# Kernel optimization log

Hardware: AMD Instinct MI355X
Metric: run time of the kernel (lower is better)

Reference implementation:

```python
import jax, jax.numpy as jnp
import numpy as np

B, H, W = 4, 64, 1024
h, w = 32, 512
K = 16
C = 64
EPS = 1e-5


def setup_inputs() -> dict:
    key = jax.random.key(0)
    ks = jax.random.split(key, 8)
    n_sampled = h * w
    xyz_proj = jax.random.normal(ks[0], (B, H, W, 3), dtype=jnp.float32)
    points_proj = jax.random.normal(ks[1], (B, H, W, C), dtype=jnp.float32)
    xyz_sampled_proj = jax.random.normal(ks[2], (B, h, w, 3), dtype=jnp.float32)
    # Precomputed neighbor selection (stand-in for fused_conv_random_k, which is
    # a non-differentiable custom CUDA op producing detached indices + mask).
    neighbor_idx = jax.random.randint(ks[3], (B, n_sampled * K), 0, H * W, dtype=jnp.int32)
    valid_mask = (jax.random.uniform(ks[4], (B, n_sampled, K, 1)) > 0.1).astype(jnp.float32)
    # 1x1 conv MLP params (torch Conv2d weight (out,in,1,1) stored here as (in,out))
    def mk(k, cin, cout):
        kw, = jax.random.split(k, 1)
        wgt = jax.random.normal(kw, (cin, cout), dtype=jnp.float32) * (1.0 / np.sqrt(cin))
        return wgt
    w0 = mk(ks[5], 3 + C, 64)
    w1 = mk(ks[6], 64, 64)
    w2 = mk(ks[7], 64, 128)
    z = lambda c: jnp.zeros((c,), jnp.float32)
    o = lambda c: jnp.ones((c,), jnp.float32)
    return dict(
        xyz_proj=xyz_proj, points_proj=points_proj, xyz_sampled_proj=xyz_sampled_proj,
        neighbor_idx=neighbor_idx, valid_mask=valid_mask,
        w0=w0, b0=z(64), g0=o(64), be0=z(64), m0=z(64), v0=o(64),
        w1=w1, b1=z(64), g1=o(64), be1=z(64), m1=z(64), v1=o(64),
        w2=w2, b2=z(128), g2=o(128), be2=z(128), m2=z(128), v2=o(128),
    )


def _conv_bn_relu(x, wgt, b, g, be, m, v):
    # 1x1 conv == matmul over channel dim; BN in eval mode with running stats.
    y = jnp.einsum('bnkc,co->bnko', x, wgt) + b
    y = g * (y - m) * jax.lax.rsqrt(v + EPS) + be
    return jax.nn.relu(y)


def reference(xyz_proj, points_proj, xyz_sampled_proj, neighbor_idx, valid_mask,
              w0, b0, g0, be0, m0, v0,
              w1, b1, g1, be1, m1, v1,
              w2, b2, g2, be2, m2, v2):
    Bc = xyz_proj.shape[0]
    Cc = points_proj.shape[3]
    hh, ww = xyz_sampled_proj.shape[1], xyz_sampled_proj.shape[2]
    n_sampled = hh * ww
    xyz_bn3 = xyz_proj.reshape(Bc, -1, 3)          # (B, H*W, 3)
    points_bnc = points_proj.reshape(Bc, -1, Cc)   # (B, H*W, C)
    idx = neighbor_idx[..., None]                  # (B, n*K, 1)
    new_xyz_group = jnp.take_along_axis(xyz_bn3, idx, axis=1).reshape(Bc, n_sampled, K, 3)
    new_points_group = jnp.take_along_axis(points_bnc, idx, axis=1).reshape(Bc, n_sampled, K, Cc)
    new_xyz_group = new_xyz_group * valid_mask
    new_points_group = new_points_group * valid_mask
    new_xyz = xyz_sampled_proj.reshape(Bc, n_sampled, 1, 3)
    xyz_diff = new_xyz_group - new_xyz             # broadcast over K
    feat = jnp.concatenate([xyz_diff, new_points_group], axis=-1)  # (B, n, K, 3+C)
    feat = _conv_bn_relu(feat, w0, b0, g0, be0, m0, v0)
    feat = _conv_bn_relu(feat, w1, b1, g1, be1, m1, v1)
    feat = _conv_bn_relu(feat, w2, b2, g2, be2, m2, v2)
    points_down_sample = jnp.max(feat, axis=2)     # (B, n, 128) max-pool over K
    points_down_sample_proj = points_down_sample.reshape(Bc, hh, ww, -1)
    return points_down_sample, points_down_sample_proj
```

## Files before the change

kernel.cpp:

```cpp
#include <hip/hip_runtime.h>


#define NGRP_    16384
#define OUTHALF_ 8388608
#define WS_      72
#define XS2_     36
#define EPS_     1e-5f
#define GRID_    1024

typedef _Float16 h8    __attribute__((ext_vector_type(8)));
typedef float    f32x4 __attribute__((ext_vector_type(4)));
typedef unsigned u32x2 __attribute__((ext_vector_type(2)));

__global__ __launch_bounds__(256) void cvt_pts_kernel(
    const float* __restrict__ src, _Float16* __restrict__ dst)
{
    const size_t i = ((size_t)blockIdx.x * 256 + threadIdx.x) * 8;
    f32x4 a = *(const f32x4*)(src + i);
    f32x4 b = *(const f32x4*)(src + i + 4);
    h8 o;
#pragma unroll
    for (int j = 0; j < 4; ++j) { o[j] = (_Float16)a[j]; o[4 + j] = (_Float16)b[j]; }
    *(h8*)(dst + i) = o;
}

#define PK(lo, hi) ({                                                          \
    const _Float16 _l = (_Float16)fmaxf((lo), 0.f);                            \
    const _Float16 _h = (_Float16)fmaxf((hi), 0.f);                            \
    (unsigned)__builtin_bit_cast(unsigned short, _l) |                         \
    ((unsigned)__builtin_bit_cast(unsigned short, _h) << 16); })

template<bool PRE>
__device__ __forceinline__ void load_pt(const void* __restrict__ ptsv,
                                        size_t row, int quad, h8& o0, h8& o1)
{
    if constexpr (PRE) {
        const _Float16* pw = (const _Float16*)ptsv + (row << 6);
        o0 = *(const h8*)(pw + quad * 8);
        o1 = *(const h8*)(pw + 32 + quad * 8);
    } else {
        const float* pw = (const float*)ptsv + (row << 6);
        f32x4 r0 = *(const f32x4*)(pw + quad * 8);
        f32x4 r1 = *(const f32x4*)(pw + quad * 8 + 4);
        f32x4 r2 = *(const f32x4*)(pw + 32 + quad * 8);
        f32x4 r3 = *(const f32x4*)(pw + 32 + quad * 8 + 4);
#pragma unroll
        for (int j = 0; j < 4; ++j) { o0[j]=(_Float16)r0[j]; o0[4+j]=(_Float16)r1[j];
                                      o1[j]=(_Float16)r2[j]; o1[4+j]=(_Float16)r3[j]; }
    }
}

template<bool PRE>
__global__ __launch_bounds__(256, 4) void pnsa_main(
    const float* __restrict__ xyz,
    const void*  __restrict__ ptsv,
    const float* __restrict__ xyzs,
    const int*   __restrict__ nidx,
    const float* __restrict__ vmask,
    const float* __restrict__ w0, const float* __restrict__ b0,
    const float* __restrict__ g0, const float* __restrict__ be0,
    const float* __restrict__ m0, const float* __restrict__ v0,
    const float* __restrict__ w1, const float* __restrict__ b1,
    const float* __restrict__ g1, const float* __restrict__ be1,
    const float* __restrict__ m1, const float* __restrict__ v1,
    const float* __restrict__ w2, const float* __restrict__ b2,
    const float* __restrict__ g2, const float* __restrict__ be2,
    const float* __restrict__ m2, const float* __restrict__ v2,
    float*       __restrict__ out)
{
    __shared__ __align__(16) _Float16 ldsW1[64 * WS_];
    __shared__ __align__(16) _Float16 ldsW2[128 * WS_];
    __shared__ __align__(16) float    t1sh[64];
    __shared__ __align__(16) float    t2sh[128];
    __shared__ __align__(16) unsigned ldsX[4][16 * XS2_];

    const int tid  = threadIdx.x;
    const int wave = tid >> 6;
    const int lane = tid & 63;
    const int l15  = lane & 15;
    const int quad = lane >> 4;

    unsigned* Xp = &ldsX[wave][0];

    if (tid < 64) {
        const float s = g1[tid] * rsqrtf(v1[tid] + EPS_);
        t1sh[tid] = (b1[tid] - m1[tid]) * s + be1[tid];
    }
    if (tid < 128) {
        const float s = g2[tid] * rsqrtf(v2[tid] + EPS_);
        t2sh[tid] = (b2[tid] - m2[tid]) * s + be2[tid];
    }
    for (int idx = tid; idx < 64 * 64; idx += 256) {
        const int k = idx >> 6, n = idx & 63;
        ldsW1[n * WS_ + k] = (_Float16)(w1[idx] * (g1[n] * rsqrtf(v1[n] + EPS_)));
    }
    for (int idx = tid; idx < 64 * 128; idx += 256) {
        const int k = idx >> 7, n = idx & 127;
        ldsW2[n * WS_ + k] = (_Float16)(w2[idx] * (g2[n] * rsqrtf(v2[n] + EPS_)));
    }
    __syncthreads();

    h8 b0f[4][3];
#pragma unroll
    for (int nt = 0; nt < 4; ++nt) {
        const int ch = nt * 16 + l15;
        const float s = g0[ch] * rsqrtf(v0[ch] + EPS_);
        const float t0 = (b0[ch] - m0[ch]) * s + be0[ch];
#pragma unroll
        for (int kk = 0; kk < 3; ++kk) {
            h8 f;
#pragma unroll
            for (int j = 0; j < 8; ++j) {
                const int k = kk * 32 + quad * 8 + j;
                float wv = 0.f;
                if (k < 64)       wv = w0[(3 + k) * 64 + ch] * s;
                else if (k < 67)  wv = w0[(k - 64) * 64 + ch] * s;
                else if (k == 67) wv = t0;
                f[j] = (_Float16)wv;
            }
            b0f[nt][kk] = f;
        }
    }

    h8 q0, q1;
    float xg0, xg1, xg2, xs0, xs1, xs2, mk;
    int nb_nxt;
    {
        const int p = (blockIdx.x << 2) + wave;
        const int nb0 = nidx[(p << 4) + l15];
        const size_t row = (size_t)(((p >> 14) << 16) + nb0);
        load_pt<PRE>(ptsv, row, quad, q0, q1);
        const float* xgp = xyz + row * 3;
        xg0 = xgp[0]; xg1 = xgp[1]; xg2 = xgp[2];
        mk = vmask[(p << 4) + l15];
        const float* xsp = xyzs + (size_t)p * 3;
        xs0 = xsp[0]; xs1 = xsp[1]; xs2 = xsp[2];
        const int g1i = (blockIdx.x + GRID_ < NGRP_) ? blockIdx.x + GRID_ : blockIdx.x;
        nb_nxt = nidx[(((g1i << 2) + wave) << 4) + l15];
    }

    for (int grp = blockIdx.x; grp < NGRP_; grp += GRID_) {
        const int p = (grp << 2) + wave;
        const int gn  = (grp + GRID_ < NGRP_) ? grp + GRID_ : grp;
        const int gnn = (gn + GRID_ < NGRP_) ? gn + GRID_ : gn;
        const int pn  = (gn << 2) + wave;

        const size_t rowN = (size_t)(((pn >> 14) << 16) + nb_nxt);
        h8 q0n, q1n;
        load_pt<PRE>(ptsv, rowN, quad, q0n, q1n);
        const float* xgpn = xyz + rowN * 3;
        const float xg0n = xgpn[0], xg1n = xgpn[1], xg2n = xgpn[2];
        const float mkn = vmask[(pn << 4) + l15];
        const float* xspn = xyzs + (size_t)pn * 3;
        const float xs0n = xspn[0], xs1n = xspn[1], xs2n = xspn[2];
        const int nb_n2 = nidx[(((gnn << 2) + wave) << 4) + l15];

        h8 a0 = q0, a1 = q1;
        if (mk == 0.0f) { a0 = (h8)(_Float16)0.f; a1 = (h8)(_Float16)0.f; }
        h8 a2 = (h8)(_Float16)0.f;
        if (quad == 0) {
            a2[0] = (_Float16)(xg0 * mk - xs0);
            a2[1] = (_Float16)(xg1 * mk - xs1);
            a2[2] = (_Float16)(xg2 * mk - xs2);
            a2[3] = (_Float16)1.0f;
        }

#pragma unroll
        for (int nt = 0; nt < 4; ++nt) {
            f32x4 acc = {0.f, 0.f, 0.f, 0.f};
            acc = __builtin_amdgcn_mfma_f32_16x16x32_f16(b0f[nt][0], a0, acc, 0, 0, 0);
            acc = __builtin_amdgcn_mfma_f32_16x16x32_f16(b0f[nt][1], a1, acc, 0, 0, 0);
            acc = __builtin_amdgcn_mfma_f32_16x16x32_f16(b0f[nt][2], a2, acc, 0, 0, 0);
            u32x2 pk = {PK(acc[0], acc[1]), PK(acc[2], acc[3])};
            *(u32x2*)(Xp + l15 * XS2_ + nt * 8 + quad * 2) = pk;
        }

        h8 x0 = *(const h8*)(Xp + l15 * XS2_ + quad * 4);
        h8 x1 = *(const h8*)(Xp + l15 * XS2_ + 16 + quad * 4);
#pragma unroll 2
        for (int nt = 0; nt < 4; ++nt) {
            const _Float16* wrow = ldsW1 + (nt * 16 + l15) * WS_ + quad * 8;
            h8 wa = *(const h8*)(wrow);
            h8 wb = *(const h8*)(wrow + 32);
            const f32x4 t1 = *(const f32x4*)(t1sh + nt * 16 + quad * 4);
            f32x4 acc = t1;
            acc = __builtin_amdgcn_mfma_f32_16x16x32_f16(wa, x0, acc, 0, 0, 0);
            acc = __builtin_amdgcn_mfma_f32_16x16x32_f16(wb, x1, acc, 0, 0, 0);
            u32x2 pk = {PK(acc[0], acc[1]), PK(acc[2], acc[3])};
            *(u32x2*)(Xp + l15 * XS2_ + nt * 8 + quad * 2) = pk;
        }

        h8 y0 = *(const h8*)(Xp + l15 * XS2_ + quad * 4);
        h8 y1 = *(const h8*)(Xp + l15 * XS2_ + 16 + quad * 4);
        float* ob = out + ((size_t)p << 7);
#pragma unroll 2
        for (int nt = 0; nt < 8; ++nt) {
            const _Float16* wrow = ldsW2 + (nt * 16 + l15) * WS_ + quad * 8;
            h8 wa = *(const h8*)(wrow);
            h8 wb = *(const h8*)(wrow + 32);
            const float t2 = t2sh[nt * 16 + l15];
            f32x4 acc = {0.f, 0.f, 0.f, 0.f};
            acc = __builtin_amdgcn_mfma_f32_16x16x32_f16(y0, wa, acc, 0, 0, 0);
            acc = __builtin_amdgcn_mfma_f32_16x16x32_f16(y1, wb, acc, 0, 0, 0);
            float v = fmaxf(fmaxf(acc[0], acc[1]), fmaxf(acc[2], acc[3])) + t2;
            v = fmaxf(v, 0.f);
            v = fmaxf(v, __shfl_xor(v, 16, 64));
            v = fmaxf(v, __shfl_xor(v, 32, 64));
            if (quad == 0) {
                ob[nt * 16 + l15]            = v;
                ob[OUTHALF_ + nt * 16 + l15] = v;
            }
        }

        q0 = q0n; q1 = q1n;
        xg0 = xg0n; xg1 = xg1n; xg2 = xg2n;
        xs0 = xs0n; xs1 = xs1n; xs2 = xs2n;
        mk = mkn; nb_nxt = nb_n2;
    }
}

extern "C" void kernel_launch(void* const* d_in, const int* in_sizes, int n_in,
                              void* d_out, int out_size, void* d_ws, size_t ws_size,
                              hipStream_t stream) {
    const float* xyz   = (const float*)d_in[0];
    const float* pts   = (const float*)d_in[1];
    const float* xyzs  = (const float*)d_in[2];
    const int*   nidx  = (const int*)d_in[3];
    const float* vmask = (const float*)d_in[4];
    const float *w0 = (const float*)d_in[5],  *b0 = (const float*)d_in[6],
                *g0 = (const float*)d_in[7],  *be0 = (const float*)d_in[8],
                *m0 = (const float*)d_in[9],  *v0 = (const float*)d_in[10];
    const float *w1 = (const float*)d_in[11], *b1 = (const float*)d_in[12],
                *g1 = (const float*)d_in[13], *be1 = (const float*)d_in[14],
                *m1 = (const float*)d_in[15], *v1 = (const float*)d_in[16];
    const float *w2 = (const float*)d_in[17], *b2 = (const float*)d_in[18],
                *g2 = (const float*)d_in[19], *be2 = (const float*)d_in[20],
                *m2 = (const float*)d_in[21], *v2 = (const float*)d_in[22];
    float* outp = (float*)d_out;

    const size_t PTS_ELEMS = 16777216ull;
    if (ws_size >= PTS_ELEMS * sizeof(_Float16)) {
        _Float16* ptsh = (_Float16*)d_ws;
        cvt_pts_kernel<<<dim3(8192), dim3(256), 0, stream>>>(pts, ptsh);
        pnsa_main<true><<<dim3(GRID_), dim3(256), 0, stream>>>(
            xyz, (const void*)ptsh, xyzs, nidx, vmask,
            w0, b0, g0, be0, m0, v0,
            w1, b1, g1, be1, m1, v1,
            w2, b2, g2, be2, m2, v2, outp);
    } else {
        pnsa_main<false><<<dim3(GRID_), dim3(256), 0, stream>>>(
            xyz, (const void*)pts, xyzs, nidx, vmask,
            w0, b0, g0, be0, m0, v0,
            w1, b1, g1, be1, m1, v1,
            w2, b2, g2, be2, m2, v2, outp);
    }
}
```

Baseline: 227.6 us.

## Hoist layer-1/2 weight fragments into registers and drop point-data software prefetch

Loads all W1/W2 MFMA fragments and bias vectors from LDS into registers once per block instead of re-reading them every group iteration. To make room, it drops the one-iteration-ahead prefetch of gathered point and xyz data (only the neighbor index is still prefetched), lowers launch bounds to 2 blocks per CU and halves the persistent grid. It also replaces the manual fp16 packing with the packed cvt_pkrtz conversion and precomputes BN scales once in shared memory. The trade is fewer LDS reads per group against lower occupancy and less latency hiding for the random gather loads.

```diff
diff --git a/kernel.cpp b/kernel.cpp
--- a/kernel.cpp
+++ b/kernel.cpp
@@ -6,9 +6,10 @@
 #define WS_      72
 #define XS2_     36
 #define EPS_     1e-5f
-#define GRID_    1024
+#define GRID_    512
 
 typedef _Float16 h8    __attribute__((ext_vector_type(8)));
+typedef _Float16 h2    __attribute__((ext_vector_type(2)));
 typedef float    f32x4 __attribute__((ext_vector_type(4)));
 typedef unsigned u32x2 __attribute__((ext_vector_type(2)));
 
@@ -24,34 +25,11 @@
     *(h8*)(dst + i) = o;
 }
 
-#define PK(lo, hi) ({                                                          \
-    const _Float16 _l = (_Float16)fmaxf((lo), 0.f);                            \
-    const _Float16 _h = (_Float16)fmaxf((hi), 0.f);                            \
-    (unsigned)__builtin_bit_cast(unsigned short, _l) |                         \
-    ((unsigned)__builtin_bit_cast(unsigned short, _h) << 16); })
+#define PK2(lo, hi) __builtin_bit_cast(unsigned,                               \
+    __builtin_amdgcn_cvt_pkrtz(fmaxf((lo), 0.f), fmaxf((hi), 0.f)))
 
 template<bool PRE>
-__device__ __forceinline__ void load_pt(const void* __restrict__ ptsv,
-                                        size_t row, int quad, h8& o0, h8& o1)
-{
-    if constexpr (PRE) {
-        const _Float16* pw = (const _Float16*)ptsv + (row << 6);
-        o0 = *(const h8*)(pw + quad * 8);
-        o1 = *(const h8*)(pw + 32 + quad * 8);
-    } else {
-        const float* pw = (const float*)ptsv + (row << 6);
-        f32x4 r0 = *(const f32x4*)(pw + quad * 8);
-        f32x4 r1 = *(const f32x4*)(pw + quad * 8 + 4);
-        f32x4 r2 = *(const f32x4*)(pw + 32 + quad * 8);
-        f32x4 r3 = *(const f32x4*)(pw + 32 + quad * 8 + 4);
-#pragma unroll
-        for (int j = 0; j < 4; ++j) { o0[j]=(_Float16)r0[j]; o0[4+j]=(_Float16)r1[j];
-                                      o1[j]=(_Float16)r2[j]; o1[4+j]=(_Float16)r3[j]; }
-    }
-}
-
-template<bool PRE>
-__global__ __launch_bounds__(256, 4) void pnsa_main(
+__global__ __launch_bounds__(256, 2) void pnsa_main(
     const float* __restrict__ xyz,
     const void*  __restrict__ ptsv,
     const float* __restrict__ xyzs,
@@ -70,8 +48,8 @@
 {
     __shared__ __align__(16) _Float16 ldsW1[64 * WS_];
     __shared__ __align__(16) _Float16 ldsW2[128 * WS_];
-    __shared__ __align__(16) float    t1sh[64];
-    __shared__ __align__(16) float    t2sh[128];
+    __shared__ __align__(16) float    s1sh[64], t1sh[64];
+    __shared__ __align__(16) float    s2sh[128], t2sh[128];
     __shared__ __align__(16) unsigned ldsX[4][16 * XS2_];
 
     const int tid  = threadIdx.x;
@@ -84,21 +62,45 @@
 
     if (tid < 64) {
         const float s = g1[tid] * rsqrtf(v1[tid] + EPS_);
+        s1sh[tid] = s;
         t1sh[tid] = (b1[tid] - m1[tid]) * s + be1[tid];
     }
     if (tid < 128) {
         const float s = g2[tid] * rsqrtf(v2[tid] + EPS_);
+        s2sh[tid] = s;
         t2sh[tid] = (b2[tid] - m2[tid]) * s + be2[tid];
     }
+    __syncthreads();
     for (int idx = tid; idx < 64 * 64; idx += 256) {
         const int k = idx >> 6, n = idx & 63;
-        ldsW1[n * WS_ + k] = (_Float16)(w1[idx] * (g1[n] * rsqrtf(v1[n] + EPS_)));
+        ldsW1[n * WS_ + k] = (_Float16)(w1[idx] * s1sh[n]);
     }
     for (int idx = tid; idx < 64 * 128; idx += 256) {
         const int k = idx >> 7, n = idx & 127;
-        ldsW2[n * WS_ + k] = (_Float16)(w2[idx] * (g2[n] * rsqrtf(v2[n] + EPS_)));
+        ldsW2[n * WS_ + k] = (_Float16)(w2[idx] * s2sh[n]);
     }
     __syncthreads();
+
+    h8 w1f[4][2], w2f[8][2];
+#pragma unroll
+    for (int nt = 0; nt < 4; ++nt) {
+        const _Float16* wrow = ldsW1 + (nt * 16 + l15) * WS_ + quad * 8;
+        w1f[nt][0] = *(const h8*)(wrow);
+        w1f[nt][1] = *(const h8*)(wrow + 32);
+    }
+#pragma unroll
+    for (int nt = 0; nt < 8; ++nt) {
+        const _Float16* wrow = ldsW2 + (nt * 16 + l15) * WS_ + quad * 8;
+        w2f[nt][0] = *(const h8*)(wrow);
+        w2f[nt][1] = *(const h8*)(wrow + 32);
+    }
+    f32x4 t1v[4];
+#pragma unroll
+    for (int nt = 0; nt < 4; ++nt)
+        t1v[nt] = *(const f32x4*)(t1sh + nt * 16 + quad * 4);
+    float t2v[8];
+#pragma unroll
+    for (int nt = 0; nt < 8; ++nt) t2v[nt] = t2sh[nt * 16 + l15];
 
     h8 b0f[4][3];
 #pragma unroll
@@ -122,41 +124,37 @@
         }
     }
 
-    h8 q0, q1;
-    float xg0, xg1, xg2, xs0, xs1, xs2, mk;
-    int nb_nxt;
-    {
-        const int p = (blockIdx.x << 2) + wave;
-        const int nb0 = nidx[(p << 4) + l15];
-        const size_t row = (size_t)(((p >> 14) << 16) + nb0);
-        load_pt<PRE>(ptsv, row, quad, q0, q1);
-        const float* xgp = xyz + row * 3;
-        xg0 = xgp[0]; xg1 = xgp[1]; xg2 = xgp[2];
-        mk = vmask[(p << 4) + l15];
-        const float* xsp = xyzs + (size_t)p * 3;
-        xs0 = xsp[0]; xs1 = xsp[1]; xs2 = xsp[2];
-        const int g1i = (blockIdx.x + GRID_ < NGRP_) ? blockIdx.x + GRID_ : blockIdx.x;
-        nb_nxt = nidx[(((g1i << 2) + wave) << 4) + l15];
-    }
+    int nb = nidx[((((blockIdx.x) << 2) + wave) << 4) + l15];
 
     for (int grp = blockIdx.x; grp < NGRP_; grp += GRID_) {
         const int p = (grp << 2) + wave;
-        const int gn  = (grp + GRID_ < NGRP_) ? grp + GRID_ : grp;
-        const int gnn = (gn + GRID_ < NGRP_) ? gn + GRID_ : gn;
-        const int pn  = (gn << 2) + wave;
-
-        const size_t rowN = (size_t)(((pn >> 14) << 16) + nb_nxt);
-        h8 q0n, q1n;
-        load_pt<PRE>(ptsv, rowN, quad, q0n, q1n);
-        const float* xgpn = xyz + rowN * 3;
-        const float xg0n = xgpn[0], xg1n = xgpn[1], xg2n = xgpn[2];
-        const float mkn = vmask[(pn << 4) + l15];
-        const float* xspn = xyzs + (size_t)pn * 3;
-        const float xs0n = xspn[0], xs1n = xspn[1], xs2n = xspn[2];
-        const int nb_n2 = nidx[(((gnn << 2) + wave) << 4) + l15];
-
-        h8 a0 = q0, a1 = q1;
-        if (mk == 0.0f) { a0 = (h8)(_Float16)0.f; a1 = (h8)(_Float16)0.f; }
+        const int gn = (grp + GRID_ < NGRP_) ? grp + GRID_ : grp;
+        const int pn = (gn << 2) + wave;
+
+        const size_t row = (size_t)(((p >> 14) << 16) + nb);
+        h8 q0, q1;
+        if constexpr (PRE) {
+            const _Float16* pw = (const _Float16*)ptsv + (row << 6);
+            q0 = *(const h8*)(pw + quad * 8);
+            q1 = *(const h8*)(pw + 32 + quad * 8);
+        } else {
+            const float* pw = (const float*)ptsv + (row << 6);
+            f32x4 r0 = *(const f32x4*)(pw + quad * 8);
+            f32x4 r1 = *(const f32x4*)(pw + quad * 8 + 4);
+            f32x4 r2 = *(const f32x4*)(pw + 32 + quad * 8);
+            f32x4 r3 = *(const f32x4*)(pw + 32 + quad * 8 + 4);
+#pragma unroll
+            for (int j = 0; j < 4; ++j) { q0[j]=(_Float16)r0[j]; q0[4+j]=(_Float16)r1[j];
+                                          q1[j]=(_Float16)r2[j]; q1[4+j]=(_Float16)r3[j]; }
+        }
+        const float mk = vmask[(p << 4) + l15];
+        const float* xgp = xyz + row * 3;
+        const float xg0 = xgp[0], xg1 = xgp[1], xg2 = xgp[2];
+        const float* xsp = xyzs + (size_t)p * 3;
+        const float xs0 = xsp[0], xs1 = xsp[1], xs2 = xsp[2];
+        const int nb_n = nidx[(pn << 4) + l15];
+
+        if (mk == 0.0f) { q0 = (h8)(_Float16)0.f; q1 = (h8)(_Float16)0.f; }
         h8 a2 = (h8)(_Float16)0.f;
         if (quad == 0) {
             a2[0] = (_Float16)(xg0 * mk - xs0);
@@ -168,41 +166,33 @@
 #pragma unroll
         for (int nt = 0; nt < 4; ++nt) {
             f32x4 acc = {0.f, 0.f, 0.f, 0.f};
-            acc = __builtin_amdgcn_mfma_f32_16x16x32_f16(b0f[nt][0], a0, acc, 0, 0, 0);
-            acc = __builtin_amdgcn_mfma_f32_16x16x32_f16(b0f[nt][1], a1, acc, 0, 0, 0);
+            acc = __builtin_amdgcn_mfma_f32_16x16x32_f16(b0f[nt][0], q0, acc, 0, 0, 0);
+            acc = __builtin_amdgcn_mfma_f32_16x16x32_f16(b0f[nt][1], q1, acc, 0, 0, 0);
             acc = __builtin_amdgcn_mfma_f32_16x16x32_f16(b0f[nt][2], a2, acc, 0, 0, 0);
-            u32x2 pk = {PK(acc[0], acc[1]), PK(acc[2], acc[3])};
+            u32x2 pk = {PK2(acc[0], acc[1]), PK2(acc[2], acc[3])};
             *(u32x2*)(Xp + l15 * XS2_ + nt * 8 + quad * 2) = pk;
         }
 
         h8 x0 = *(const h8*)(Xp + l15 * XS2_ + quad * 4);
         h8 x1 = *(const h8*)(Xp + l15 * XS2_ + 16 + quad * 4);
-#pragma unroll 2
+#pragma unroll
         for (int nt = 0; nt < 4; ++nt) {
-            const _Float16* wrow = ldsW1 + (nt * 16 + l15) * WS_ + quad * 8;
-            h8 wa = *(const h8*)(wrow);
-            h8 wb = *(const h8*)(wrow + 32);
-            const f32x4 t1 = *(const f32x4*)(t1sh + nt * 16 + quad * 4);
-            f32x4 acc = t1;
-            acc = __builtin_amdgcn_mfma_f32_16x16x32_f16(wa, x0, acc, 0, 0, 0);
-            acc = __builtin_amdgcn_mfma_f32_16x16x32_f16(wb, x1, acc, 0, 0, 0);
-            u32x2 pk = {PK(acc[0], acc[1]), PK(acc[2], acc[3])};
+            f32x4 acc = t1v[nt];
+            acc = __builtin_amdgcn_mfma_f32_16x16x32_f16(w1f[nt][0], x0, acc, 0, 0, 0);
+            acc = __builtin_amdgcn_mfma_f32_16x16x32_f16(w1f[nt][1], x1, acc, 0, 0, 0);
+            u32x2 pk = {PK2(acc[0], acc[1]), PK2(acc[2], acc[3])};
             *(u32x2*)(Xp + l15 * XS2_ + nt * 8 + quad * 2) = pk;
         }
 
         h8 y0 = *(const h8*)(Xp + l15 * XS2_ + quad * 4);
         h8 y1 = *(const h8*)(Xp + l15 * XS2_ + 16 + quad * 4);
         float* ob = out + ((size_t)p << 7);
-#pragma unroll 2
+#pragma unroll
         for (int nt = 0; nt < 8; ++nt) {
-            const _Float16* wrow = ldsW2 + (nt * 16 + l15) * WS_ + quad * 8;
-            h8 wa = *(const h8*)(wrow);
-            h8 wb = *(const h8*)(wrow + 32);
-            const float t2 = t2sh[nt * 16 + l15];
             f32x4 acc = {0.f, 0.f, 0.f, 0.f};
-            acc = __builtin_amdgcn_mfma_f32_16x16x32_f16(y0, wa, acc, 0, 0, 0);
-            acc = __builtin_amdgcn_mfma_f32_16x16x32_f16(y1, wb, acc, 0, 0, 0);
-            float v = fmaxf(fmaxf(acc[0], acc[1]), fmaxf(acc[2], acc[3])) + t2;
+            acc = __builtin_amdgcn_mfma_f32_16x16x32_f16(y0, w2f[nt][0], acc, 0, 0, 0);
+            acc = __builtin_amdgcn_mfma_f32_16x16x32_f16(y1, w2f[nt][1], acc, 0, 0, 0);
+            float v = fmaxf(fmaxf(acc[0], acc[1]), fmaxf(acc[2], acc[3])) + t2v[nt];
             v = fmaxf(v, 0.f);
             v = fmaxf(v, __shfl_xor(v, 16, 64));
             v = fmaxf(v, __shfl_xor(v, 32, 64));
@@ -212,10 +202,7 @@
             }
         }
 
-        q0 = q0n; q1 = q1n;
-        xg0 = xg0n; xg1 = xg1n; xg2 = xg2n;
-        xs0 = xs0n; xs1 = xs1n; xs2 = xs2n;
-        mk = mkn; nb_nxt = nb_n2;
+        nb = nb_n;
     }
 }
 
```

Measured after the change: 243.2 us. 6.8% more time.
